# Optimization experiments

Measured on AMD Instinct MI355X. Metric: run time of the kernel, lower is better.

Reference implementation:

```python
import jax, jax.numpy as jnp
import numpy as np

B, N, H, D, L = 4, 1024, 8, 256, 4
SVD, NSP = 16, 512
DK = D // H
EPS = 1e-6


def setup_inputs() -> dict:
    key = jax.random.key(0)
    ks = jax.random.split(key, 40)
    p = {}
    p["x"] = jax.random.normal(ks[0], (B, N, D), jnp.float32)
    p["in_degrees"] = jax.random.randint(ks[1], (N,), 0, N)
    p["out_degrees"] = jax.random.randint(ks[2], (N,), 0, N)
    p["spatial_pos"] = jax.random.randint(ks[3], (N, N), 0, NSP)
    p["svd_emb"] = jax.random.normal(ks[4], (N, 2 * SVD), jnp.float32)
    # embedding tables (padding_idx=0 -> zero row)
    p["in_deg_emb"] = (0.02 * jax.random.normal(ks[5], (N, D), jnp.float32)).at[0].set(0.0)
    p["out_deg_emb"] = (0.02 * jax.random.normal(ks[6], (N, D), jnp.float32)).at[0].set(0.0)
    p["spatial_emb"] = (0.02 * jax.random.normal(ks[7], (NSP, H), jnp.float32)).at[0].set(0.0)
    # SVD linear (stored [in, out]; y = x @ W + b)
    p["W_svd"] = 0.02 * jax.random.normal(ks[8], (2 * SVD, D), jnp.float32)
    p["b_svd"] = jnp.zeros((D,), jnp.float32)
    # per-layer stacked transformer params
    names = ["Wq", "Wk", "Wv", "Wa", "W1", "W2"]
    for i, nm in enumerate(names):
        p[nm] = 0.05 * jax.random.normal(ks[9 + i], (L, D, D), jnp.float32)
    for nm in ["bq", "bk", "bv", "ba", "b1", "b2", "ln1_b", "ln2_b"]:
        p[nm] = jnp.zeros((L, D), jnp.float32)
    p["ln1_g"] = jnp.ones((L, D), jnp.float32)
    p["ln2_g"] = jnp.ones((L, D), jnp.float32)
    return p


def _ln(x, g, b):
    mu = jnp.mean(x, axis=-1, keepdims=True)
    var = jnp.mean(jnp.square(x - mu), axis=-1, keepdims=True)
    return (x - mu) * jax.lax.rsqrt(var + EPS) * g + b


def _forward(x, svd_emb, W_svd, b_svd, in_deg_emb, out_deg_emb, spatial_emb,
             Wq, bq, Wk, bk, Wv, bv, Wa, ba, ln1_g, ln1_b,
             W1, b1, W2, b2, ln2_g, ln2_b,
             in_degrees, out_degrees, spatial_pos):
    # node-level: degree embeddings ([N,D] broadcasts over batch)
    x = x + in_deg_emb[in_degrees] + out_deg_emb[out_degrees]
    # node-level: SVD embedding (deterministic sign = +1 -> concat(u, -v))
    pos = jnp.concatenate([svd_emb[:, :SVD], -svd_emb[:, SVD:]], axis=-1)
    x = x + pos @ W_svd + b_svd
    # attention-level spatial bias: [N,N,H] -> [H,N,N], broadcast over batch
    attn_bias = jnp.transpose(spatial_emb[spatial_pos], (2, 0, 1))
    scale = 1.0 / jnp.sqrt(jnp.asarray(DK, x.dtype))

    def body(h, params):
        wq, bq_, wk, bk_, wv, bv_, wa, ba_, g1, b1_, w1, bb1, w2, bb2, g2, b2_ = params
        q = (h @ wq + bq_).reshape(B, N, H, DK)
        k = (h @ wk + bk_).reshape(B, N, H, DK)
        v = (h @ wv + bv_).reshape(B, N, H, DK)
        # scores [B,H,N,N] + spatial bias [H,N,N]
        scores = jnp.einsum('bqhd,bkhd->bhqk', q, k) * scale + attn_bias
        attn = jax.nn.softmax(scores, axis=-1)
        o = jnp.einsum('bhqk,bkhd->bqhd', attn, v).reshape(B, N, D)
        h = _ln(h + o @ wa + ba_, g1, b1_)
        f = jnp.maximum(h @ w1 + bb1, 0.0) @ w2 + bb2
        h = _ln(h + f, g2, b2_)
        return h, None

    x, _ = jax.lax.scan(body, x, (Wq, bq, Wk, bk, Wv, bv, Wa, ba, ln1_g, ln1_b,
                                  W1, b1, W2, b2, ln2_g, ln2_b))
    return x


def reference(x, svd_emb, W_svd, b_svd, in_deg_emb, out_deg_emb, spatial_emb,
              Wq, bq, Wk, bk, Wv, bv, Wa, ba, ln1_g, ln1_b,
              W1, b1, W2, b2, ln2_g, ln2_b,
              in_degrees, out_degrees, spatial_pos):
    return _forward(x, svd_emb, W_svd, b_svd, in_deg_emb, out_deg_emb, spatial_emb,
                    Wq, bq, Wk, bk, Wv, bv, Wa, ba, ln1_g, ln1_b,
                    W1, b1, W2, b2, ln2_g, ln2_b,
                    in_degrees, out_degrees, spatial_pos)
```

## Files before the change

### kernel.cpp

```cpp
#include <hip/hip_runtime.h>
#include <hip/hip_bf16.h>
#include <math.h>

#define NN 1024
#define BB 4
#define HH 8
#define DD 256
#define LL 4
#define DKK 32
#define MM 4096
#define EPSF 1e-6f

typedef __attribute__((ext_vector_type(8))) short short8;
typedef __attribute__((ext_vector_type(4))) float f32x4;

__device__ __forceinline__ unsigned short f2bf(float f) {
    __hip_bfloat16 h = __float2bfloat16(f);
    return *(unsigned short*)&h;
}
__device__ __forceinline__ float bf2f(unsigned short u) {
    unsigned v = ((unsigned)u) << 16;
    return __builtin_bit_cast(float, v);
}

__global__ __launch_bounds__(256) void init_kernel(
    const float* __restrict__ x, const int* __restrict__ deg_in,
    const int* __restrict__ deg_out, const float* __restrict__ svd,
    const float* __restrict__ in_emb, const float* __restrict__ out_emb,
    const float* __restrict__ Wsvd, const float* __restrict__ bsvd,
    const float* __restrict__ Wq, const float* __restrict__ Wk,
    const float* __restrict__ Wv, const float* __restrict__ Wa,
    const float* __restrict__ W1, const float* __restrict__ W2,
    const int* __restrict__ sp, const float* __restrict__ spemb,
    float* __restrict__ h, short* __restrict__ hb,
    short* __restrict__ Wt, short* __restrict__ bsw)
{
    int blk = blockIdx.x;
    int tid = threadIdx.x;
    {
        int n = blk & (NN - 1);
        int di = deg_in[n], dou = deg_out[n];
        float acc = x[(size_t)blk * DD + tid] + in_emb[(size_t)di * DD + tid]
                  + out_emb[(size_t)dou * DD + tid] + bsvd[tid];
        const float* sv = &svd[n * 32];
#pragma unroll
        for (int j = 0; j < 32; ++j) {
            float v = sv[j];
            v = (j < 16) ? v : -v;
            acc += v * Wsvd[j * DD + tid];
        }
        h[(size_t)blk * DD + tid] = acc;
        hb[(size_t)blk * DD + tid] = (short)f2bf(acc);
    }
    if (blk < 384) {
        __shared__ float t[64][65];
        int z = blk >> 4, tile = blk & 15;
        int name = z >> 2;
        const float* srcs[6] = {Wq, Wk, Wv, Wa, W1, W2};
        const float* W = srcs[name] + (size_t)(z & 3) * DD * DD;
        short* dst = Wt + (size_t)z * DD * DD;
        int r0 = (tile >> 2) * 64, c0 = (tile & 3) * 64;
#pragma unroll
        for (int i = 0; i < 16; ++i) {
            int idx = i * 256 + tid;
            int r = idx >> 6, cc = idx & 63;
            t[r][cc] = W[(size_t)(r0 + r) * DD + c0 + cc];
        }
        __syncthreads();
#pragma unroll
        for (int i = 0; i < 16; ++i) {
            int idx = i * 256 + tid;
            int n = idx >> 6, k = idx & 63;
            dst[(size_t)(c0 + n) * DD + r0 + k] = (short)f2bf(t[k][n]);
        }
    } else if (blk < 640) {
        int tt = (blk - 384) * 256 + tid;
        int ln = tt & 63, kt = (tt >> 6) & 15, q16 = tt >> 10;
        int qd = ln >> 4, cc = ln & 15;
        unsigned buf[8][8];
#pragma unroll
        for (int j = 0; j < 16; ++j) {
            int f = j >> 2, r = j & 3;
            int row = q16 * 16 + qd * 4 + r;
            int col = kt * 64 + f * 16 + cc;
            int pp = sp[row * NN + col];
#pragma unroll
            for (int hh = 0; hh < 8; ++hh) {
                unsigned short u = f2bf(spemb[pp * 8 + hh]);
                if (j & 1) buf[hh][j >> 1] |= ((unsigned)u) << 16;
                else       buf[hh][j >> 1] = u;
            }
        }
#pragma unroll
        for (int hh = 0; hh < 8; ++hh) {
            uint4* dst = (uint4*)&bsw[(((size_t)hh * 64 + q16) * 16 + kt) * 1024 + (size_t)ln * 16];
            dst[0] = make_uint4(buf[hh][0], buf[hh][1], buf[hh][2], buf[hh][3]);
            dst[1] = make_uint4(buf[hh][4], buf[hh][5], buf[hh][6], buf[hh][7]);
        }
    }
}

__global__ __launch_bounds__(256) void gemm_qkv_kernel(
    const short* __restrict__ A,
    const short* __restrict__ Wtq, const short* __restrict__ Wtk,
    const short* __restrict__ Wtv,
    const float* __restrict__ bq, const float* __restrict__ bk,
    const float* __restrict__ bv,
    short* __restrict__ qo, short* __restrict__ ko, short* __restrict__ vo)
{
    int z = blockIdx.z;
    const short* Wt = (z == 0) ? Wtq : (z == 1) ? Wtk : Wtv;
    const float* bs = (z == 0) ? bq : (z == 1) ? bk : bv;
    int tid = threadIdx.x, wave = tid >> 6, lane = tid & 63;
    int quad = lane >> 4, c = lane & 15;
    int m0 = blockIdx.x * 16;
    int n0 = blockIdx.y * 64 + wave * 16;
    f32x4 acc = {0.f, 0.f, 0.f, 0.f};
    const short* Ap = &A[(size_t)(m0 + c) * DD];
#pragma unroll
    for (int ks = 0; ks < 8; ++ks) {
        short8 af = *(const short8*)&Ap[ks * 32 + quad * 8];
        short8 bf = *(const short8*)&Wt[(size_t)(n0 + c) * DD + ks * 32 + quad * 8];
        acc = __builtin_amdgcn_mfma_f32_16x16x32_bf16(af, bf, acc, 0, 0, 0);
    }
    int b = m0 >> 10;
    int tok0 = (m0 & (NN - 1)) + quad * 4;
    int col = n0 + c;
    int head = col >> 5, dk = col & 31;
    int bh = b * 8 + head;
    float bv2 = bs[col];
    const float scale = 0.17677669529663687f;
    if (z == 2) {
        ushort4 pk;
        pk.x = f2bf(acc[0] + bv2); pk.y = f2bf(acc[1] + bv2);
        pk.z = f2bf(acc[2] + bv2); pk.w = f2bf(acc[3] + bv2);
        *(ushort4*)&vo[((size_t)bh * DKK + dk) * NN + tok0] = pk;
    } else {
        short* out = (z == 0) ? qo : ko;
        float sc = (z == 0) ? scale : 1.0f;
#pragma unroll
        for (int r = 0; r < 4; ++r)
            out[((size_t)bh * NN + tok0 + r) * DKK + dk] =
                (short)f2bf((acc[r] + bv2) * sc);
    }
}

__global__ __launch_bounds__(256) void attn_kernel(
    const short* __restrict__ q, const short* __restrict__ k,
    const short* __restrict__ vt, const short* __restrict__ bsw,
    short* __restrict__ o)
{
    int bh = blockIdx.y;
    int b = bh >> 3, h = bh & 7;
    int t = blockIdx.x;
    int tid = threadIdx.x, wave = tid >> 6, lane = tid & 63;
    int quad = lane >> 4, c = lane & 15;
    int q0 = t * 16;
    __shared__ short Pl[4][16][72];
    __shared__ float Om[4][16][32];
    __shared__ float Ml[4][16][2];
    short (*P)[72] = Pl[wave];
    short8 qf = *(const short8*)&q[((size_t)bh * NN + q0 + c) * DKK + quad * 8];
    float m_i[4], l_i[4];
    f32x4 Oa0 = {0.f, 0.f, 0.f, 0.f};
    f32x4 Oa1 = {0.f, 0.f, 0.f, 0.f};
#pragma unroll
    for (int r = 0; r < 4; ++r) { m_i[r] = -1e30f; l_i[r] = 0.f; }
    const f32x4 zero = {0.f, 0.f, 0.f, 0.f};
#pragma unroll
    for (int j = 0; j < 4; ++j) {
        int kti = wave * 4 + j;
        int kt = kti * 64;
        f32x4 s[4];
#pragma unroll
        for (int f = 0; f < 4; ++f) {
            short8 kf = *(const short8*)&k[((size_t)bh * NN + kt + f * 16 + c) * DKK + quad * 8];
            s[f] = __builtin_amdgcn_mfma_f32_16x16x32_bf16(qf, kf, zero, 0, 0, 0);
        }
        const short* bp = &bsw[(((size_t)h * 64 + t) * 16 + kti) * 1024 + (size_t)lane * 16];
        short8 b0 = *(const short8*)bp;
        short8 b1 = *(const short8*)(bp + 8);
#pragma unroll
        for (int f = 0; f < 4; ++f)
#pragma unroll
            for (int r = 0; r < 4; ++r) {
                int jj = f * 4 + r;
                unsigned short uu = (unsigned short)((jj < 8) ? b0[jj] : b1[jj - 8]);
                s[f][r] += bf2f(uu);
            }
#pragma unroll
        for (int r = 0; r < 4; ++r) {
            float mt2 = fmaxf(fmaxf(s[0][r], s[1][r]), fmaxf(s[2][r], s[3][r]));
#pragma unroll
            for (int off = 1; off < 16; off <<= 1) mt2 = fmaxf(mt2, __shfl_xor(mt2, off));
            float mn = fmaxf(m_i[r], mt2);
            float alpha = __expf(m_i[r] - mn);
            m_i[r] = mn;
            float rs = 0.f;
#pragma unroll
            for (int f = 0; f < 4; ++f) {
                float pr = __expf(s[f][r] - mn);
                s[f][r] = pr;
                rs += pr;
            }
#pragma unroll
            for (int off = 1; off < 16; off <<= 1) rs += __shfl_xor(rs, off);
            l_i[r] = l_i[r] * alpha + rs;
            Oa0[r] *= alpha;
            Oa1[r] *= alpha;
        }
#pragma unroll
        for (int f = 0; f < 4; ++f)
#pragma unroll
            for (int r = 0; r < 4; ++r)
                P[quad * 4 + r][f * 16 + c] = (short)f2bf(s[f][r]);
#pragma unroll
        for (int kc = 0; kc < 2; ++kc) {
            short8 pf = *(const short8*)&P[c][kc * 32 + quad * 8];
            short8 vf0 = *(const short8*)&vt[((size_t)bh * DKK + 0  + c) * NN + kt + kc * 32 + quad * 8];
            short8 vf1 = *(const short8*)&vt[((size_t)bh * DKK + 16 + c) * NN + kt + kc * 32 + quad * 8];
            Oa0 = __builtin_amdgcn_mfma_f32_16x16x32_bf16(pf, vf0, Oa0, 0, 0, 0);
            Oa1 = __builtin_amdgcn_mfma_f32_16x16x32_bf16(pf, vf1, Oa1, 0, 0, 0);
        }
    }
    if (c == 0)
#pragma unroll
        for (int r = 0; r < 4; ++r) {
            Ml[wave][quad * 4 + r][0] = m_i[r];
            Ml[wave][quad * 4 + r][1] = l_i[r];
        }
#pragma unroll
    for (int r = 0; r < 4; ++r) {
        Om[wave][quad * 4 + r][c]      = Oa0[r];
        Om[wave][quad * 4 + r][16 + c] = Oa1[r];
    }
    __syncthreads();
    int row = tid >> 4;
    float mg = fmaxf(fmaxf(Ml[0][row][0], Ml[1][row][0]),
                     fmaxf(Ml[2][row][0], Ml[3][row][0]));
    float sc[4], lg = 0.f;
#pragma unroll
    for (int w = 0; w < 4; ++w) {
        sc[w] = __expf(Ml[w][row][0] - mg);
        lg += Ml[w][row][1] * sc[w];
    }
    float invl = 1.0f / lg;
    int col0 = (tid & 15) * 2;
    float o0 = 0.f, o1 = 0.f;
#pragma unroll
    for (int w = 0; w < 4; ++w) {
        o0 += Om[w][row][col0] * sc[w];
        o1 += Om[w][row][col0 + 1] * sc[w];
    }
    ushort2 pk;
    pk.x = f2bf(o0 * invl);
    pk.y = f2bf(o1 * invl);
    *(ushort2*)&o[((size_t)b * NN + q0 + row) * DD + h * DKK + col0] = pk;
}

__global__ __launch_bounds__(256) void post_kernel(
    const short* __restrict__ obb,
    const short* __restrict__ Wta, const short* __restrict__ Wt1,
    const short* __restrict__ Wt2,
    const float* __restrict__ ba, const float* __restrict__ b1,
    const float* __restrict__ b2,
    const float* __restrict__ g1, const float* __restrict__ lb1,
    const float* __restrict__ g2, const float* __restrict__ lb2,
    float* __restrict__ h, short* __restrict__ hb)
{
    int tid = threadIdx.x, wave = tid >> 6, lane = tid & 63;
    int quad = lane >> 4, c = lane & 15;
    int m0 = blockIdx.x * 16;

    __shared__ short t_in[16][264];
    __shared__ short t1s[16][264];
    __shared__ float shs[4][16][2];
    const f32x4 zero = {0.f, 0.f, 0.f, 0.f};

    f32x4 acc[4] = {zero, zero, zero, zero};
    {
        const short* Ap = &obb[(size_t)(m0 + c) * DD];
#pragma unroll
        for (int ks = 0; ks < 8; ++ks) {
            short8 af = *(const short8*)&Ap[ks * 32 + quad * 8];
#pragma unroll
            for (int f = 0; f < 4; ++f) {
                short8 bf = *(const short8*)&Wta[(size_t)(wave * 64 + f * 16 + c) * DD + ks * 32 + quad * 8];
                acc[f] = __builtin_amdgcn_mfma_f32_16x16x32_bf16(af, bf, acc[f], 0, 0, 0);
            }
        }
    }
    float val[4][4];
    float ps[4] = {0.f,0.f,0.f,0.f}, ps2[4] = {0.f,0.f,0.f,0.f};
#pragma unroll
    for (int f = 0; f < 4; ++f) {
        int col = wave * 64 + f * 16 + c;
        float bv = ba[col];
#pragma unroll
        for (int r = 0; r < 4; ++r) {
            float v = h[(size_t)(m0 + quad * 4 + r) * DD + col] + acc[f][r] + bv;
            val[f][r] = v;
            ps[r] += v;
            ps2[r] += v * v;
        }
    }
#pragma unroll
    for (int r = 0; r < 4; ++r)
#pragma unroll
        for (int off = 1; off < 16; off <<= 1) {
            ps[r]  += __shfl_xor(ps[r], off);
            ps2[r] += __shfl_xor(ps2[r], off);
        }
    if (c == 0)
#pragma unroll
        for (int r = 0; r < 4; ++r) {
            shs[wave][quad * 4 + r][0] = ps[r];
            shs[wave][quad * 4 + r][1] = ps2[r];
        }
    __syncthreads();
    float res[4][4];
#pragma unroll
    for (int r = 0; r < 4; ++r) {
        int rr = quad * 4 + r;
        float ts = shs[0][rr][0] + shs[1][rr][0] + shs[2][rr][0] + shs[3][rr][0];
        float t2 = shs[0][rr][1] + shs[1][rr][1] + shs[2][rr][1] + shs[3][rr][1];
        float mu = ts * (1.0f / DD);
        float rv = rsqrtf(t2 * (1.0f / DD) - mu * mu + EPSF);
#pragma unroll
        for (int f = 0; f < 4; ++f) {
            int col = wave * 64 + f * 16 + c;
            float nv = (val[f][r] - mu) * rv * g1[col] + lb1[col];
            res[f][r] = nv;
            h[(size_t)(m0 + rr) * DD + col] = nv;
            short bfv = (short)f2bf(nv);
            hb[(size_t)(m0 + rr) * DD + col] = bfv;
            t_in[rr][col] = bfv;
        }
    }
    __syncthreads();
#pragma unroll
    for (int f = 0; f < 4; ++f) {
        int n0 = wave * 64 + f * 16;
        f32x4 a1 = zero;
#pragma unroll
        for (int ks = 0; ks < 8; ++ks) {
            short8 af = *(const short8*)&t_in[c][ks * 32 + quad * 8];
            short8 bf = *(const short8*)&Wt1[(size_t)(n0 + c) * DD + ks * 32 + quad * 8];
            a1 = __builtin_amdgcn_mfma_f32_16x16x32_bf16(af, bf, a1, 0, 0, 0);
        }
        float bv = b1[n0 + c];
#pragma unroll
        for (int r = 0; r < 4; ++r)
            t1s[quad * 4 + r][n0 + c] = (short)f2bf(fmaxf(a1[r] + bv, 0.f));
    }
    __syncthreads();
    f32x4 acc2[4] = {zero, zero, zero, zero};
#pragma unroll
    for (int ks = 0; ks < 8; ++ks) {
        short8 af = *(const short8*)&t1s[c][ks * 32 + quad * 8];
#pragma unroll
        for (int f = 0; f < 4; ++f) {
            short8 bf = *(const short8*)&Wt2[(size_t)(wave * 64 + f * 16 + c) * DD + ks * 32 + quad * 8];
            acc2[f] = __builtin_amdgcn_mfma_f32_16x16x32_bf16(af, bf, acc2[f], 0, 0, 0);
        }
    }
    float ps_2[4] = {0.f,0.f,0.f,0.f}, ps2_2[4] = {0.f,0.f,0.f,0.f};
#pragma unroll
    for (int f = 0; f < 4; ++f) {
        int col = wave * 64 + f * 16 + c;
        float bv = b2[col];
#pragma unroll
        for (int r = 0; r < 4; ++r) {
            float v = res[f][r] + acc2[f][r] + bv;
            val[f][r] = v;
            ps_2[r] += v;
            ps2_2[r] += v * v;
        }
    }
#pragma unroll
    for (int r = 0; r < 4; ++r)
#pragma unroll
        for (int off = 1; off < 16; off <<= 1) {
            ps_2[r]  += __shfl_xor(ps_2[r], off);
            ps2_2[r] += __shfl_xor(ps2_2[r], off);
        }
    __syncthreads();
    if (c == 0)
#pragma unroll
        for (int r = 0; r < 4; ++r) {
            shs[wave][quad * 4 + r][0] = ps_2[r];
            shs[wave][quad * 4 + r][1] = ps2_2[r];
        }
    __syncthreads();
#pragma unroll
    for (int r = 0; r < 4; ++r) {
        int rr = quad * 4 + r;
        float ts = shs[0][rr][0] + shs[1][rr][0] + shs[2][rr][0] + shs[3][rr][0];
        float t2 = shs[0][rr][1] + shs[1][rr][1] + shs[2][rr][1] + shs[3][rr][1];
        float mu = ts * (1.0f / DD);
        float rv = rsqrtf(t2 * (1.0f / DD) - mu * mu + EPSF);
#pragma unroll
        for (int f = 0; f < 4; ++f) {
            int col = wave * 64 + f * 16 + c;
            float nv = (val[f][r] - mu) * rv * g2[col] + lb2[col];
            h[(size_t)(m0 + rr) * DD + col] = nv;
            hb[(size_t)(m0 + rr) * DD + col] = (short)f2bf(nv);
        }
    }
}

extern "C" void kernel_launch(void* const* d_in, const int* in_sizes, int n_in,
                              void* d_out, int out_size, void* d_ws, size_t ws_size,
                              hipStream_t stream)
{
    const float* x       = (const float*)d_in[0];
    const int*   deg_in  = (const int*)d_in[1];
    const int*   deg_out = (const int*)d_in[2];
    const int*   sp      = (const int*)d_in[3];
    const float* svd     = (const float*)d_in[4];
    const float* in_emb  = (const float*)d_in[5];
    const float* out_emb = (const float*)d_in[6];
    const float* spemb   = (const float*)d_in[7];
    const float* Wsvd    = (const float*)d_in[8];
    const float* bsvd    = (const float*)d_in[9];
    const float* Wq = (const float*)d_in[10];
    const float* Wk = (const float*)d_in[11];
    const float* Wv = (const float*)d_in[12];
    const float* Wa = (const float*)d_in[13];
    const float* W1 = (const float*)d_in[14];
    const float* W2 = (const float*)d_in[15];
    const float* bq = (const float*)d_in[16];
    const float* bk = (const float*)d_in[17];
    const float* bv = (const float*)d_in[18];
    const float* ba = (const float*)d_in[19];
    const float* b1 = (const float*)d_in[20];
    const float* b2 = (const float*)d_in[21];
    const float* ln1b = (const float*)d_in[22];
    const float* ln2b = (const float*)d_in[23];
    const float* ln1g = (const float*)d_in[24];
    const float* ln2g = (const float*)d_in[25];

    float* h = (float*)d_out;
    char*  ws = (char*)d_ws;
    short* bias = (short*)ws;
    short* qb   = (short*)(ws + ((size_t)16 << 20));
    short* kb   = (short*)(ws + ((size_t)18 << 20));
    short* vtb  = (short*)(ws + ((size_t)20 << 20));
    short* obb  = (short*)(ws + ((size_t)22 << 20));
    short* hb   = (short*)(ws + ((size_t)26 << 20));
    short* Wt   = (short*)(ws + ((size_t)28 << 20));

    init_kernel<<<MM, 256, 0, stream>>>(x, deg_in, deg_out, svd, in_emb,
        out_emb, Wsvd, bsvd, Wq, Wk, Wv, Wa, W1, W2, sp, spemb, h, hb, Wt, bias);

    const size_t WSZ = (size_t)DD * DD;
    for (int l = 0; l < LL; ++l) {
        const size_t bo = (size_t)l * DD;
        const short* Wtq = Wt + (0 * 4 + l) * WSZ;
        const short* Wtk = Wt + (1 * 4 + l) * WSZ;
        const short* Wtv = Wt + (2 * 4 + l) * WSZ;
        const short* Wta = Wt + (3 * 4 + l) * WSZ;
        const short* Wt1 = Wt + (4 * 4 + l) * WSZ;
        const short* Wt2 = Wt + (5 * 4 + l) * WSZ;

        gemm_qkv_kernel<<<dim3(MM / 16, 4, 3), 256, 0, stream>>>(
            hb, Wtq, Wtk, Wtv, bq + bo, bk + bo, bv + bo, qb, kb, vtb);
        attn_kernel<<<dim3(NN / 16, BB * HH), 256, 0, stream>>>(
            qb, kb, vtb, bias, obb);
        post_kernel<<<MM / 16, 256, 0, stream>>>(
            obb, Wta, Wt1, Wt2, ba + bo, b1 + bo, b2 + bo,
            ln1g + bo, ln1b + bo, ln2g + bo, ln2b + bo, h, hb);
    }
}
```

Before: 403.9 us.

## Fuse next layer's QKV projection into post kernel epilogue

```diff
diff --git a/kernel.cpp b/kernel.cpp
--- a/kernel.cpp
+++ b/kernel.cpp
@@ -258,6 +258,7 @@
     *(ushort2*)&o[((size_t)b * NN + q0 + row) * DD + h * DKK + col0] = pk;
 }
 
+template <int QKV>
 __global__ __launch_bounds__(256) void post_kernel(
     const short* __restrict__ obb,
     const short* __restrict__ Wta, const short* __restrict__ Wt1,
@@ -266,7 +267,12 @@
     const float* __restrict__ b2,
     const float* __restrict__ g1, const float* __restrict__ lb1,
     const float* __restrict__ g2, const float* __restrict__ lb2,
-    float* __restrict__ h, short* __restrict__ hb)
+    float* __restrict__ h, short* __restrict__ hb,
+    const short* __restrict__ Wtqn, const short* __restrict__ Wtkn,
+    const short* __restrict__ Wtvn,
+    const float* __restrict__ bqn, const float* __restrict__ bkn,
+    const float* __restrict__ bvn,
+    short* __restrict__ qo, short* __restrict__ ko, short* __restrict__ vo)
 {
     int tid = threadIdx.x, wave = tid >> 6, lane = tid & 63;
     int quad = lane >> 4, c = lane & 15;
@@ -331,7 +337,6 @@
             int col = wave * 64 + f * 16 + c;
             float nv = (val[f][r] - mu) * rv * g1[col] + lb1[col];
             res[f][r] = nv;
-            h[(size_t)(m0 + rr) * DD + col] = nv;
             short bfv = (short)f2bf(nv);
             hb[(size_t)(m0 + rr) * DD + col] = bfv;
             t_in[rr][col] = bfv;
@@ -404,7 +409,49 @@
             int col = wave * 64 + f * 16 + c;
             float nv = (val[f][r] - mu) * rv * g2[col] + lb2[col];
             h[(size_t)(m0 + rr) * DD + col] = nv;
-            hb[(size_t)(m0 + rr) * DD + col] = (short)f2bf(nv);
+            short bfv = (short)f2bf(nv);
+            hb[(size_t)(m0 + rr) * DD + col] = bfv;
+            t_in[rr][col] = bfv;
+        }
+    }
+    if (QKV == 0) return;
+    __syncthreads();
+    {
+        int b = m0 >> 10;
+        int tok0 = (m0 & (NN - 1)) + quad * 4;
+        const short* Wz[3]  = {Wtqn, Wtkn, Wtvn};
+        const float* bz[3]  = {bqn, bkn, bvn};
+        const float scale = 0.17677669529663687f;
+#pragma unroll
+        for (int z = 0; z < 3; ++z) {
+#pragma unroll
+            for (int f = 0; f < 4; ++f) {
+                int n0 = wave * 64 + f * 16;
+                f32x4 aq = zero;
+#pragma unroll
+                for (int ks = 0; ks < 8; ++ks) {
+                    short8 af = *(const short8*)&t_in[c][ks * 32 + quad * 8];
+                    short8 bf = *(const short8*)&Wz[z][(size_t)(n0 + c) * DD + ks * 32 + quad * 8];
+                    aq = __builtin_amdgcn_mfma_f32_16x16x32_bf16(af, bf, aq, 0, 0, 0);
+                }
+                int col = n0 + c;
+                int head = col >> 5, dk = col & 31;
+                int bh = b * 8 + head;
+                float bv2 = bz[z][col];
+                if (z == 2) {
+                    ushort4 pk;
+                    pk.x = f2bf(aq[0] + bv2); pk.y = f2bf(aq[1] + bv2);
+                    pk.z = f2bf(aq[2] + bv2); pk.w = f2bf(aq[3] + bv2);
+                    *(ushort4*)&vo[((size_t)bh * DKK + dk) * NN + tok0] = pk;
+                } else {
+                    short* out = (z == 0) ? qo : ko;
+                    float sc = (z == 0) ? scale : 1.0f;
+#pragma unroll
+                    for (int r = 0; r < 4; ++r)
+                        out[((size_t)bh * NN + tok0 + r) * DKK + dk] =
+                            (short)f2bf((aq[r] + bv2) * sc);
+                }
+            }
         }
     }
 }
@@ -454,21 +501,32 @@
         out_emb, Wsvd, bsvd, Wq, Wk, Wv, Wa, W1, W2, sp, spemb, h, hb, Wt, bias);
 
     const size_t WSZ = (size_t)DD * DD;
+    gemm_qkv_kernel<<<dim3(MM / 16, 4, 3), 256, 0, stream>>>(
+        hb, Wt + 0 * WSZ, Wt + 4 * WSZ, Wt + 8 * WSZ, bq, bk, bv, qb, kb, vtb);
+
     for (int l = 0; l < LL; ++l) {
         const size_t bo = (size_t)l * DD;
-        const short* Wtq = Wt + (0 * 4 + l) * WSZ;
-        const short* Wtk = Wt + (1 * 4 + l) * WSZ;
-        const short* Wtv = Wt + (2 * 4 + l) * WSZ;
         const short* Wta = Wt + (3 * 4 + l) * WSZ;
         const short* Wt1 = Wt + (4 * 4 + l) * WSZ;
         const short* Wt2 = Wt + (5 * 4 + l) * WSZ;
 
-        gemm_qkv_kernel<<<dim3(MM / 16, 4, 3), 256, 0, stream>>>(
-            hb, Wtq, Wtk, Wtv, bq + bo, bk + bo, bv + bo, qb, kb, vtb);
         attn_kernel<<<dim3(NN / 16, BB * HH), 256, 0, stream>>>(
             qb, kb, vtb, bias, obb);
-        post_kernel<<<MM / 16, 256, 0, stream>>>(
-            obb, Wta, Wt1, Wt2, ba + bo, b1 + bo, b2 + bo,
-            ln1g + bo, ln1b + bo, ln2g + bo, ln2b + bo, h, hb);
-    }
-}
+
+        if (l < LL - 1) {
+            const size_t bo_n = (size_t)(l + 1) * DD;
+            post_kernel<1><<<MM / 16, 256, 0, stream>>>(
+                obb, Wta, Wt1, Wt2, ba + bo, b1 + bo, b2 + bo,
+                ln1g + bo, ln1b + bo, ln2g + bo, ln2b + bo, h, hb,
+                Wt + (0 * 4 + l + 1) * WSZ, Wt + (1 * 4 + l + 1) * WSZ,
+                Wt + (2 * 4 + l + 1) * WSZ,
+                bq + bo_n, bk + bo_n, bv + bo_n, qb, kb, vtb);
+        } else {
+            post_kernel<0><<<MM / 16, 256, 0, stream>>>(
+                obb, Wta, Wt1, Wt2, ba + bo, b1 + bo, b2 + bo,
+                ln1g + bo, ln1b + bo, ln2g + bo, ln2b + bo, h, hb,
+                nullptr, nullptr, nullptr, nullptr, nullptr, nullptr,
+                nullptr, nullptr, nullptr);
+        }
+    }
+}
```

Measured after the change: 375.4 us. 7.0% less time.
